# Optimization experiments

Measured on AMD Instinct MI355X. Metric: run time of the kernel, lower is better.

Reference implementation:

```python
import jax, jax.numpy as jnp
import numpy as np

D_MODEL, D_Q, D_K, D_V, N = 1024, 128, 128, 128, 8192

def setup_inputs() -> dict:
    key = jax.random.key(0)
    ks = jax.random.split(key, 7)
    s = 1.0 / np.sqrt(D_MODEL)
    return {
        "x": jax.random.normal(ks[0], (N, D_MODEL), dtype=jnp.float32),
        "Wq": jax.random.uniform(ks[1], (D_MODEL, D_Q), jnp.float32, -s, s),
        "bq": jax.random.uniform(ks[2], (D_Q,), jnp.float32, -s, s),
        "Wk": jax.random.uniform(ks[3], (D_MODEL, D_K), jnp.float32, -s, s),
        "bk": jax.random.uniform(ks[4], (D_K,), jnp.float32, -s, s),
        "Wv": jax.random.uniform(ks[5], (D_MODEL, D_V), jnp.float32, -s, s),
        "bv": jax.random.uniform(ks[6], (D_V,), jnp.float32, -s, s),
    }

def reference(x, Wq, bq, Wk, bk, Wv, bv):
    q = x @ Wq + bq          # [N, d_q]
    k = x @ Wk + bk          # [N, d_k]
    v = x @ Wv + bv          # [N, d_v]
    scale = jnp.sqrt(jnp.asarray(q.shape[-1], q.dtype))
    scores = (q @ k.T) / scale          # [N, N]
    attn = jax.nn.softmax(scores, axis=1)  # matches nn.Softmax(dim=1) on 2D
    return attn @ v                     # [N, d_v]
```

## Files before the change

### kernel.cpp

```cpp
#include <hip/hip_runtime.h>


typedef __attribute__((ext_vector_type(8))) short bf16x8;
typedef __attribute__((ext_vector_type(4))) float f32x4;

#define NTOK 8192
#define DMODEL 1024
#define DH 128
#define NSPLIT 8
#define CPS 16

__device__ __forceinline__ unsigned short f2bf(float f) {
  __bf16 h = (__bf16)f;
  return __builtin_bit_cast(unsigned short, h);
}

__device__ __forceinline__ unsigned int pack2bf(float a, float b) {
  return (unsigned int)f2bf(a) | ((unsigned int)f2bf(b) << 16);
}

__device__ __forceinline__ void gl2lds16(const void* gp, void* lp) {
  const __attribute__((address_space(1))) unsigned int* g =
      (const __attribute__((address_space(1))) unsigned int*)gp;
  __attribute__((address_space(3))) unsigned int* l =
      (__attribute__((address_space(3))) unsigned int*)lp;
  __builtin_amdgcn_global_load_lds(g, l, 16, 0, 0);
}

__global__ __launch_bounds__(256) void k_build_wt(const float* __restrict__ Wq,
                                                  const float* __restrict__ Wk,
                                                  const float* __restrict__ Wv,
                                                  unsigned short* __restrict__ wt) {
  __shared__ unsigned short tile[32 * 130];
  int k0 = blockIdx.x * 32;
  int p = blockIdx.y;
  int t = threadIdx.x;
  const float* W = (p == 0) ? Wq : ((p == 1) ? Wk : Wv);
  float vscale = (p == 2) ? 0.0625f : 1.0f;
#pragma unroll
  for (int i = 0; i < 16; i++) {
    int e = i * 256 + t;
    int n = e & 127, kk = e >> 7;
    tile[kk * 130 + n] = f2bf(W[(size_t)(k0 + kk) * DH + n] * vscale);
  }
  __syncthreads();
#pragma unroll
  for (int i = 0; i < 16; i++) {
    int e = i * 256 + t;
    int kk = e & 31, n = e >> 5;
    wt[(size_t)(p * DH + n) * DMODEL + k0 + kk] = tile[kk * 130 + n];
  }
}

__global__ __launch_bounds__(256, 2) void k_qkv(const float* __restrict__ x,
                                                const unsigned short* __restrict__ wt,
                                                const float* __restrict__ bq,
                                                const float* __restrict__ bk,
                                                const float* __restrict__ bv,
                                                unsigned short* __restrict__ qs,
                                                unsigned short* __restrict__ kkv,
                                                unsigned short* __restrict__ vt) {
  __shared__ float xt[2][64 * 64];
  __shared__ unsigned short wtt[2][128 * 64];
  int mt = blockIdx.x, p = blockIdx.y;
  int tid = threadIdx.x;
  int w = tid >> 6, lane = tid & 63, l16 = lane & 15, g = lane >> 4;

#define STAGE_QKV(buf, k0)                                                     \
  {                                                                            \
    _Pragma("unroll") for (int r = 0; r < 4; r++) {                            \
      int seg = r * 4 + w;                                                     \
      int xr = seg * 4 + (lane >> 4);                                          \
      int xlc = ((lane & 15) ^ (xr & 15)) & 15;                                \
      gl2lds16(&x[(size_t)(mt * 64 + xr) * DMODEL + (k0) + xlc * 4],           \
               &xt[buf][seg * 256]);                                           \
      int wc = seg * 8 + (lane >> 3);                                          \
      int wlc = ((lane & 7) ^ (wc & 7)) & 7;                                   \
      gl2lds16(&wt[(size_t)(p * DH + wc) * DMODEL + (k0) + wlc * 8],           \
               &wtt[buf][seg * 512]);                                          \
    }                                                                          \
  }

  f32x4 zero = {0.f, 0.f, 0.f, 0.f};
  f32x4 acc[8];
#pragma unroll
  for (int i = 0; i < 8; i++) acc[i] = zero;

  STAGE_QKV(0, 0);
  STAGE_QKV(1, 64);
  int arow = w * 16 + l16;
  for (int kt2 = 0; kt2 < 16; kt2++) {
    int b = kt2 & 1;
    if (kt2 < 15)
      asm volatile("s_waitcnt vmcnt(8)\n\ts_barrier" ::: "memory");
    else
      asm volatile("s_waitcnt vmcnt(0)\n\ts_barrier" ::: "memory");

    bf16x8 a[2];
#pragma unroll
    for (int half = 0; half < 2; half++) {
      int lc0 = half * 8 + g * 2;
      const f32x4 u0 = *(const f32x4*)&xt[b][arow * 64 + ((lc0 ^ l16) & 15) * 4];
      const f32x4 u1 = *(const f32x4*)&xt[b][arow * 64 + (((lc0 + 1) ^ l16) & 15) * 4];
      union { unsigned int u[4]; bf16x8 v; } pk;
      pk.u[0] = pack2bf(u0[0], u0[1]);
      pk.u[1] = pack2bf(u0[2], u0[3]);
      pk.u[2] = pack2bf(u1[0], u1[1]);
      pk.u[3] = pack2bf(u1[2], u1[3]);
      a[half] = pk.v;
    }
#pragma unroll
    for (int nt = 0; nt < 8; nt++) {
      int col = nt * 16 + l16;
#pragma unroll
      for (int half = 0; half < 2; half++) {
        int lc = half * 4 + g;
        bf16x8 bf = *(const bf16x8*)&wtt[b][col * 64 + ((lc ^ (col & 7)) & 7) * 8];
        acc[nt] = __builtin_amdgcn_mfma_f32_16x16x32_bf16(a[half], bf, acc[nt], 0, 0, 0);
      }
    }

    asm volatile("s_waitcnt lgkmcnt(0)\n\ts_barrier" ::: "memory");
    if (kt2 + 2 < 16) STAGE_QKV(b, (kt2 + 2) * 64);
  }
#undef STAGE_QKV

  const float* bias = (p == 0) ? bq : ((p == 1) ? bk : bv);
  float mult = (p == 0) ? (0.08838834764831845f * 1.44269504088896340f) : 1.0f;
  if (p < 2) {
    unsigned short* outp = (p == 0) ? qs : kkv;
#pragma unroll
    for (int nt = 0; nt < 8; nt++) {
      int col = nt * 16 + l16;
      float bsv = bias[col];
#pragma unroll
      for (int r = 0; r < 4; r++) {
        int row = mt * 64 + w * 16 + g * 4 + r;
        outp[(size_t)row * DH + col] = f2bf((acc[nt][r] + bsv) * mult);
      }
    }
  } else {
#pragma unroll
    for (int nt = 0; nt < 8; nt++) {
      int col = nt * 16 + l16;
      float bsv = bias[col] * 0.0625f;
      int row0 = mt * 64 + w * 16 + g * 4;
      uint2 uv;
      uv.x = pack2bf(acc[nt][0] + bsv, acc[nt][1] + bsv);
      uv.y = pack2bf(acc[nt][2] + bsv, acc[nt][3] + bsv);
      *(uint2*)(&vt[(size_t)col * NTOK + row0]) = uv;
    }
  }
}

__global__ __launch_bounds__(256, 2) void k_flash(const unsigned short* __restrict__ qs,
                                                  const unsigned short* __restrict__ kkv,
                                                  const unsigned short* __restrict__ vt,
                                                  _Float16* __restrict__ opart,
                                                  float* __restrict__ lpart) {
  __shared__ unsigned short kt[2][64 * 128];
  __shared__ unsigned short vtl[2][128 * 64];
  __shared__ unsigned short pscr[4 * 2 * 1024];
  int sp = blockIdx.x, qt = blockIdx.y;
  int tid = threadIdx.x;
  int w = tid >> 6, lane = tid & 63, l16 = lane & 15, g = lane >> 4;
  int swz2 = (l16 & 7) ^ ((l16 >> 3) << 1);

  bf16x8 qf[2][4];
  int qbase = qt * 128 + w * 32;
#pragma unroll
  for (int q2 = 0; q2 < 2; q2++)
#pragma unroll
    for (int f = 0; f < 4; f++)
      qf[q2][f] = *(const bf16x8*)(&qs[(size_t)(qbase + q2 * 16 + l16) * DH + f * 32 + g * 8]);

  int pcK[4], pcV[2], pcP[2];
#pragma unroll
  for (int f = 0; f < 4; f++) {
    int lc = f * 4 + g;
    pcK[f] = (lc & 8) | ((lc ^ l16) & 7);
  }
#pragma unroll
  for (int kb = 0; kb < 2; kb++) {
    int lc = kb * 4 + g;
    pcV[kb] = (lc ^ l16) & 7;
    pcP[kb] = (lc ^ swz2) & 7;
  }

#define STAGE_FLASH(buf, chunk)                                                 \
  {                                                                             \
    int key0 = (chunk) * 64;                                                    \
    _Pragma("unroll") for (int ii = 0; ii < 4; ii++) {                          \
      int i = w * 4 + ii;                                                       \
      int krow = 4 * i + (lane >> 4);                                           \
      int klc = ((lane & 15) & 8) | (((lane & 15) ^ krow) & 7);                 \
      gl2lds16(&kkv[(size_t)(key0 + krow) * DH + klc * 8], &kt[buf][i * 512]);  \
      int vrow = 8 * i + (lane >> 3);                                           \
      int vlc = ((lane & 7) ^ vrow) & 7;                                        \
      gl2lds16(&vt[(size_t)vrow * NTOK + key0 + vlc * 8], &vtl[buf][i * 512]);  \
    }                                                                           \
  }

#define SM_TILE(m)                                                              \
  {                                                                             \
    _Pragma("unroll") for (int q2 = 0; q2 < 2; q2++) {                          \
      float p0 = __builtin_amdgcn_exp2f(s[q2][m][0]);                           \
      float p1 = __builtin_amdgcn_exp2f(s[q2][m][1]);                           \
      float p2 = __builtin_amdgcn_exp2f(s[q2][m][2]);                           \
      float p3 = __builtin_amdgcn_exp2f(s[q2][m][3]);                           \
      if (q2) ssum1 += (p0 + p1) + (p2 + p3);                                   \
      else    ssum0 += (p0 + p1) + (p2 + p3);                                   \
      uint2 uv;                                                                 \
      uv.x = pack2bf(p0, p1);                                                   \
      uv.y = pack2bf(p2, p3);                                                   \
      int ch = (((m) * 2 + (g >> 1)) ^ swz2) & 7;                               \
      *(uint2*)(&pscr[(w * 2 + q2) * 1024 + l16 * 64 + ch * 8 + (g & 1) * 4]) = uv; \
    }                                                                           \
  }

  f32x4 zero = {0.f, 0.f, 0.f, 0.f};
  f32x4 o[2][8];
#pragma unroll
  for (int q2 = 0; q2 < 2; q2++)
#pragma unroll
    for (int dt = 0; dt < 8; dt++) o[q2][dt] = zero;
  float l[2] = {0.f, 0.f};

  int c0 = sp * CPS;
  STAGE_FLASH(0, c0);
  STAGE_FLASH(1, c0 + 1);

  for (int it = 0; it < CPS; it++) {
    int b = it & 1;
    if (it < CPS - 1)
      asm volatile("s_waitcnt vmcnt(8)\n\ts_barrier" ::: "memory");
    else
      asm volatile("s_waitcnt vmcnt(0)\n\ts_barrier" ::: "memory");

    f32x4 s[2][4];
    float ssum0 = 0.f, ssum1 = 0.f;
    __builtin_amdgcn_s_setprio(1);
#pragma unroll
    for (int mt = 0; mt < 4; mt++) {
      bf16x8 kf[4];
#pragma unroll
      for (int f = 0; f < 4; f++)
        kf[f] = *(const bf16x8*)(&kt[b][(mt * 16 + l16) * 128 + pcK[f] * 8]);
      s[0][mt] = zero;
      s[1][mt] = zero;
#pragma unroll
      for (int f = 0; f < 4; f++) {
        s[0][mt] = __builtin_amdgcn_mfma_f32_16x16x32_bf16(kf[f], qf[0][f], s[0][mt], 0, 0, 0);
        s[1][mt] = __builtin_amdgcn_mfma_f32_16x16x32_bf16(kf[f], qf[1][f], s[1][mt], 0, 0, 0);
      }
      if (mt >= 1) { SM_TILE(mt - 1); }
    }
    SM_TILE(3);
    __builtin_amdgcn_s_setprio(0);
    l[0] += ssum0;
    l[1] += ssum1;

    bf16x8 pb[2][2];
#pragma unroll
    for (int q2 = 0; q2 < 2; q2++)
#pragma unroll
      for (int kb = 0; kb < 2; kb++)
        pb[q2][kb] = *(const bf16x8*)(&pscr[(w * 2 + q2) * 1024 + l16 * 64 + pcP[kb] * 8]);

    __builtin_amdgcn_s_setprio(1);
#pragma unroll
    for (int dt = 0; dt < 8; dt++)
#pragma unroll
      for (int kb = 0; kb < 2; kb++) {
        bf16x8 vf = *(const bf16x8*)(&vtl[b][(dt * 16 + l16) * 64 + pcV[kb] * 8]);
        o[0][dt] = __builtin_amdgcn_mfma_f32_16x16x32_bf16(vf, pb[0][kb], o[0][dt], 0, 0, 0);
        o[1][dt] = __builtin_amdgcn_mfma_f32_16x16x32_bf16(vf, pb[1][kb], o[1][dt], 0, 0, 0);
      }
    __builtin_amdgcn_s_setprio(0);

    asm volatile("s_waitcnt lgkmcnt(0)\n\ts_barrier" ::: "memory");
    if (it + 2 < CPS) STAGE_FLASH(b, c0 + it + 2);
  }
#undef SM_TILE
#undef STAGE_FLASH

#pragma unroll
  for (int q2 = 0; q2 < 2; q2++) {
    l[q2] += __shfl_xor(l[q2], 16);
    l[q2] += __shfl_xor(l[q2], 32);
    int qrow = qbase + q2 * 16 + l16;
    size_t obase = ((size_t)sp * NTOK + qrow) * DH;
#pragma unroll
    for (int dt = 0; dt < 8; dt++) {
      union { _Float16 h[4]; uint2 u; } pk;
      pk.h[0] = (_Float16)o[q2][dt][0];
      pk.h[1] = (_Float16)o[q2][dt][1];
      pk.h[2] = (_Float16)o[q2][dt][2];
      pk.h[3] = (_Float16)o[q2][dt][3];
      *(uint2*)(&opart[obase + dt * 16 + g * 4]) = pk.u;
    }
    if (g == 0) lpart[sp * NTOK + qrow] = l[q2];
  }
}

__global__ __launch_bounds__(256) void k_merge(const _Float16* __restrict__ opart,
                                               const float* __restrict__ lpart,
                                               float* __restrict__ out) {
  int gid = blockIdx.x * 256 + threadIdx.x;
  int row = gid >> 4, c8 = gid & 15;
  float den = 0.f;
  float n0 = 0.f, n1 = 0.f, n2 = 0.f, n3 = 0.f;
  float n4 = 0.f, n5 = 0.f, n6 = 0.f, n7 = 0.f;
#pragma unroll
  for (int s = 0; s < NSPLIT; s++) {
    den += lpart[s * NTOK + row];
    union { uint4 u; _Float16 h[8]; } v;
    v.u = *(const uint4*)&opart[((size_t)s * NTOK + row) * DH + c8 * 8];
    n0 += (float)v.h[0]; n1 += (float)v.h[1];
    n2 += (float)v.h[2]; n3 += (float)v.h[3];
    n4 += (float)v.h[4]; n5 += (float)v.h[5];
    n6 += (float)v.h[6]; n7 += (float)v.h[7];
  }
  float inv = 16.0f / den;
  size_t ob = (size_t)row * DH + c8 * 8;
  *(float4*)&out[ob]     = make_float4(n0 * inv, n1 * inv, n2 * inv, n3 * inv);
  *(float4*)&out[ob + 4] = make_float4(n4 * inv, n5 * inv, n6 * inv, n7 * inv);
}

extern "C" void kernel_launch(void* const* d_in, const int* in_sizes, int n_in,
                              void* d_out, int out_size, void* d_ws, size_t ws_size,
                              hipStream_t stream) {
  const float* x  = (const float*)d_in[0];
  const float* Wq = (const float*)d_in[1];
  const float* bq = (const float*)d_in[2];
  const float* Wk = (const float*)d_in[3];
  const float* bk = (const float*)d_in[4];
  const float* Wv = (const float*)d_in[5];
  const float* bv = (const float*)d_in[6];
  float* out = (float*)d_out;

  char* ws = (char*)d_ws;
  _Float16*       opart = (_Float16*)(ws);
  unsigned short* wt  = (unsigned short*)(ws + 16777216);
  unsigned short* qsb = (unsigned short*)(ws + 17563648);
  unsigned short* kkb = (unsigned short*)(ws + 19660800);
  unsigned short* vtb = (unsigned short*)(ws + 21757952);
  float* lpart = (float*)(ws + 23855104);

  k_build_wt<<<dim3(32, 3), 256, 0, stream>>>(Wq, Wk, Wv, wt);
  k_qkv<<<dim3(128, 3), 256, 0, stream>>>(x, wt, bq, bk, bv, qsb, kkb, vtb);
  k_flash<<<dim3(NSPLIT, 64), 256, 0, stream>>>(qsb, kkb, vtb, opart, lpart);
  k_merge<<<512, 256, 0, stream>>>(opart, lpart, out);
}
```

Measured before the change: 143.5 us.

## Fuse Q/K/V projections into one block per 32-row tile of x

The QKV projection kernel now computes all three projections in one block over a 32-row tile of x, with 8 waves each owning a 16-column slice across Q, K and V. Before, separate blocks per projection each loaded the same x tile. Each x element is now read from global memory and converted to bf16 once instead of three times. In exchange the block doubles to 512 threads, the weight LDS buffer is three times larger, occupancy drops to one block per CU, and the grid has 256 blocks instead of 384.

```diff
diff --git a/kernel.cpp b/kernel.cpp
--- a/kernel.cpp
+++ b/kernel.cpp
@@ -52,7 +52,7 @@
   }
 }
 
-__global__ __launch_bounds__(256, 2) void k_qkv(const float* __restrict__ x,
+__global__ __launch_bounds__(512, 1) void k_qkv(const float* __restrict__ x,
                                                 const unsigned short* __restrict__ wt,
                                                 const float* __restrict__ bq,
                                                 const float* __restrict__ bk,
@@ -60,94 +60,100 @@
                                                 unsigned short* __restrict__ qs,
                                                 unsigned short* __restrict__ kkv,
                                                 unsigned short* __restrict__ vt) {
-  __shared__ float xt[2][64 * 64];
-  __shared__ unsigned short wtt[2][128 * 64];
-  int mt = blockIdx.x, p = blockIdx.y;
+  __shared__ float xt[2][32 * 64];
+  __shared__ unsigned short wtt[2][3][128 * 64];
+  int mt = blockIdx.x;
   int tid = threadIdx.x;
   int w = tid >> 6, lane = tid & 63, l16 = lane & 15, g = lane >> 4;
 
 #define STAGE_QKV(buf, k0)                                                     \
   {                                                                            \
-    _Pragma("unroll") for (int r = 0; r < 4; r++) {                            \
-      int seg = r * 4 + w;                                                     \
-      int xr = seg * 4 + (lane >> 4);                                          \
-      int xlc = ((lane & 15) ^ (xr & 15)) & 15;                                \
-      gl2lds16(&x[(size_t)(mt * 64 + xr) * DMODEL + (k0) + xlc * 4],           \
-               &xt[buf][seg * 256]);                                           \
+    int xr = w * 4 + (lane >> 4);                                              \
+    int xlc = ((lane & 15) ^ (xr & 15)) & 15;                                  \
+    gl2lds16(&x[(size_t)(mt * 32 + xr) * DMODEL + (k0) + xlc * 4],             \
+             &xt[buf][w * 256]);                                               \
+    _Pragma("unroll") for (int r = 0; r < 6; r++) {                            \
+      int gseg = w * 6 + r;                                                    \
+      int pp = gseg >> 4, seg = gseg & 15;                                     \
       int wc = seg * 8 + (lane >> 3);                                          \
       int wlc = ((lane & 7) ^ (wc & 7)) & 7;                                   \
-      gl2lds16(&wt[(size_t)(p * DH + wc) * DMODEL + (k0) + wlc * 8],           \
-               &wtt[buf][seg * 512]);                                          \
+      gl2lds16(&wt[(size_t)(pp * DH + wc) * DMODEL + (k0) + wlc * 8],          \
+               &wtt[buf][pp][seg * 512]);                                      \
     }                                                                          \
   }
 
   f32x4 zero = {0.f, 0.f, 0.f, 0.f};
-  f32x4 acc[8];
-#pragma unroll
-  for (int i = 0; i < 8; i++) acc[i] = zero;
+  f32x4 acc[3][2];
+#pragma unroll
+  for (int p = 0; p < 3; p++)
+#pragma unroll
+    for (int m = 0; m < 2; m++) acc[p][m] = zero;
 
   STAGE_QKV(0, 0);
   STAGE_QKV(1, 64);
-  int arow = w * 16 + l16;
+  int col = w * 16 + l16;
   for (int kt2 = 0; kt2 < 16; kt2++) {
     int b = kt2 & 1;
     if (kt2 < 15)
-      asm volatile("s_waitcnt vmcnt(8)\n\ts_barrier" ::: "memory");
+      asm volatile("s_waitcnt vmcnt(7)\n\ts_barrier" ::: "memory");
     else
       asm volatile("s_waitcnt vmcnt(0)\n\ts_barrier" ::: "memory");
 
-    bf16x8 a[2];
-#pragma unroll
-    for (int half = 0; half < 2; half++) {
-      int lc0 = half * 8 + g * 2;
-      const f32x4 u0 = *(const f32x4*)&xt[b][arow * 64 + ((lc0 ^ l16) & 15) * 4];
-      const f32x4 u1 = *(const f32x4*)&xt[b][arow * 64 + (((lc0 + 1) ^ l16) & 15) * 4];
-      union { unsigned int u[4]; bf16x8 v; } pk;
-      pk.u[0] = pack2bf(u0[0], u0[1]);
-      pk.u[1] = pack2bf(u0[2], u0[3]);
-      pk.u[2] = pack2bf(u1[0], u1[1]);
-      pk.u[3] = pack2bf(u1[2], u1[3]);
-      a[half] = pk.v;
+    bf16x8 a[2][2];
+#pragma unroll
+    for (int m = 0; m < 2; m++) {
+      int arow = m * 16 + l16;
+#pragma unroll
+      for (int half = 0; half < 2; half++) {
+        int lc0 = half * 8 + g * 2;
+        const f32x4 u0 = *(const f32x4*)&xt[b][arow * 64 + ((lc0 ^ l16) & 15) * 4];
+        const f32x4 u1 = *(const f32x4*)&xt[b][arow * 64 + (((lc0 + 1) ^ l16) & 15) * 4];
+        union { unsigned int u[4]; bf16x8 v; } pk;
+        pk.u[0] = pack2bf(u0[0], u0[1]);
+        pk.u[1] = pack2bf(u0[2], u0[3]);
+        pk.u[2] = pack2bf(u1[0], u1[1]);
+        pk.u[3] = pack2bf(u1[2], u1[3]);
+        a[m][half] = pk.v;
+      }
     }
 #pragma unroll
-    for (int nt = 0; nt < 8; nt++) {
-      int col = nt * 16 + l16;
+    for (int p = 0; p < 3; p++)
 #pragma unroll
       for (int half = 0; half < 2; half++) {
         int lc = half * 4 + g;
-        bf16x8 bf = *(const bf16x8*)&wtt[b][col * 64 + ((lc ^ (col & 7)) & 7) * 8];
-        acc[nt] = __builtin_amdgcn_mfma_f32_16x16x32_bf16(a[half], bf, acc[nt], 0, 0, 0);
-      }
-    }
+        bf16x8 bf = *(const bf16x8*)&wtt[b][p][col * 64 + ((lc ^ (col & 7)) & 7) * 8];
+        acc[p][0] = __builtin_amdgcn_mfma_f32_16x16x32_bf16(a[0][half], bf, acc[p][0], 0, 0, 0);
+        acc[p][1] = __builtin_amdgcn_mfma_f32_16x16x32_bf16(a[1][half], bf, acc[p][1], 0, 0, 0);
+      }
 
     asm volatile("s_waitcnt lgkmcnt(0)\n\ts_barrier" ::: "memory");
     if (kt2 + 2 < 16) STAGE_QKV(b, (kt2 + 2) * 64);
   }
 #undef STAGE_QKV
 
-  const float* bias = (p == 0) ? bq : ((p == 1) ? bk : bv);
-  float mult = (p == 0) ? (0.08838834764831845f * 1.44269504088896340f) : 1.0f;
-  if (p < 2) {
+  const float qmult = 0.08838834764831845f * 1.44269504088896340f;
+#pragma unroll
+  for (int p = 0; p < 2; p++) {
+    const float* bias = (p == 0) ? bq : bk;
     unsigned short* outp = (p == 0) ? qs : kkv;
-#pragma unroll
-    for (int nt = 0; nt < 8; nt++) {
-      int col = nt * 16 + l16;
-      float bsv = bias[col];
+    float mult = (p == 0) ? qmult : 1.0f;
+    float bsv = bias[col];
+#pragma unroll
+    for (int m = 0; m < 2; m++)
 #pragma unroll
       for (int r = 0; r < 4; r++) {
-        int row = mt * 64 + w * 16 + g * 4 + r;
-        outp[(size_t)row * DH + col] = f2bf((acc[nt][r] + bsv) * mult);
-      }
-    }
-  } else {
-#pragma unroll
-    for (int nt = 0; nt < 8; nt++) {
-      int col = nt * 16 + l16;
-      float bsv = bias[col] * 0.0625f;
-      int row0 = mt * 64 + w * 16 + g * 4;
+        int row = mt * 32 + m * 16 + g * 4 + r;
+        outp[(size_t)row * DH + col] = f2bf((acc[p][m][r] + bsv) * mult);
+      }
+  }
+  {
+    float bsv = bv[col] * 0.0625f;
+#pragma unroll
+    for (int m = 0; m < 2; m++) {
+      int row0 = mt * 32 + m * 16 + g * 4;
       uint2 uv;
-      uv.x = pack2bf(acc[nt][0] + bsv, acc[nt][1] + bsv);
-      uv.y = pack2bf(acc[nt][2] + bsv, acc[nt][3] + bsv);
+      uv.x = pack2bf(acc[2][m][0] + bsv, acc[2][m][1] + bsv);
+      uv.y = pack2bf(acc[2][m][2] + bsv, acc[2][m][3] + bsv);
       *(uint2*)(&vt[(size_t)col * NTOK + row0]) = uv;
     }
   }
@@ -348,7 +354,7 @@
   float* lpart = (float*)(ws + 23855104);
 
   k_build_wt<<<dim3(32, 3), 256, 0, stream>>>(Wq, Wk, Wv, wt);
-  k_qkv<<<dim3(128, 3), 256, 0, stream>>>(x, wt, bq, bk, bv, qsb, kkb, vtb);
+  k_qkv<<<dim3(256), 512, 0, stream>>>(x, wt, bq, bk, bv, qsb, kkb, vtb);
   k_flash<<<dim3(NSPLIT, 64), 256, 0, stream>>>(qsb, kkb, vtb, opart, lpart);
   k_merge<<<512, 256, 0, stream>>>(opart, lpart, out);
 }
```

Result: no change. 145.8 us (+1.6%).
